# Optimization experiments

Hardware: AMD Instinct MI355X
Metric: run time of the kernel (lower is better)

## Reference

```python
import jax, jax.numpy as jnp
import numpy as np

N_NODES = 10000
N_EDGES = 160000
IN_FEATS = 512
H_FEATS = 512
NUM_CLASSES = 128


def setup_inputs() -> dict:
    key = jax.random.key(0)
    ks = jax.random.split(key, 7)
    h = jax.random.normal(ks[0], (N_NODES, IN_FEATS), dtype=jnp.float32)
    W1 = jax.random.normal(ks[1], (2 * IN_FEATS, H_FEATS), dtype=jnp.float32) * 0.02
    b1 = jax.random.normal(ks[2], (H_FEATS,), dtype=jnp.float32) * 0.02
    W2 = jax.random.normal(ks[3], (2 * H_FEATS, NUM_CLASSES), dtype=jnp.float32) * 0.02
    b2 = jax.random.normal(ks[4], (NUM_CLASSES,), dtype=jnp.float32) * 0.02
    src = jax.random.randint(ks[5], (N_EDGES,), 0, N_NODES, dtype=jnp.int32)
    dst = jax.random.randint(ks[6], (N_EDGES,), 0, N_NODES, dtype=jnp.int32)
    return {"h": h, "W1": W1, "b1": b1, "W2": W2, "b2": b2, "src": src, "dst": dst}


def _weighted_sage_conv(h, W, b, src, dst, n_nodes):
    # message = u_mul_e('h','w') with w == ones -> just gather source features
    msg = h[src]  # [E, d]
    # fn.mean reduce at destination: segment-sum / in-degree (0 if no in-edges)
    s = jax.ops.segment_sum(msg, dst, num_segments=n_nodes)  # [N, d]
    cnt = jax.ops.segment_sum(jnp.ones((src.shape[0],), h.dtype), dst, num_segments=n_nodes)
    h_N = s / jnp.maximum(cnt, 1.0)[:, None]
    h_total = jnp.concatenate([h, h_N], axis=1)  # [N, 2d]
    return h_total @ W + b


def reference(h, W1, b1, W2, b2, src, dst):
    n = h.shape[0]
    h1 = jax.nn.relu(_weighted_sage_conv(h, W1, b1, src, dst, n))
    return _weighted_sage_conv(h1, W2, b2, src, dst, n)
```

## Files before the change

### kernel.cpp

```cpp
#include <hip/hip_runtime.h>

typedef unsigned short u16;
typedef unsigned char u8;
typedef __attribute__((ext_vector_type(2))) float floatx2;
typedef __attribute__((ext_vector_type(4))) float floatx4;
typedef __attribute__((ext_vector_type(8))) __bf16 bf16x8;
typedef __attribute__((ext_vector_type(2))) unsigned short us2;
typedef __attribute__((ext_vector_type(4))) unsigned short us4;
typedef __attribute__((ext_vector_type(8))) unsigned short us8;
typedef __attribute__((ext_vector_type(2))) unsigned int u32x2;

static __device__ __forceinline__ float b2f(u16 v) {
    union { unsigned u; float f; } x; x.u = ((unsigned)v) << 16; return x.f;
}
static __device__ __forceinline__ u16 f2b(float f) {
    union { float f; unsigned u; } x; x.f = f;
    unsigned u = x.u;
    return (u16)((u + 0x7fffu + ((u >> 16) & 1u)) >> 16);
}

#define GLOAD_LDS16(g, l) __builtin_amdgcn_global_load_lds( \
    (const __attribute__((address_space(1))) void*)(g),     \
    (__attribute__((address_space(3))) void*)(l), 16, 0, 0)

#define CAP 64
#define SPILLMAX 4096

static __device__ __forceinline__ int detect_blk(const u16* __restrict__ p,
                                                 int nelem, int* sh) {
    if (threadIdx.x == 0) *sh = 0;
    __syncthreads();
    const int lim = nelem < 512 ? nelem : 512;
    int found = 0;
    for (int j = threadIdx.x; 2 * j < lim; j += 256) {
        unsigned v = p[2 * j] & 0x7fffu;
        if (v >= 0x4280u) found = 1;
    }
    if (found) atomicOr(sh, 1);
    __syncthreads();
    return *sh;
}

__global__ __launch_bounds__(256) void k_d1(
    const int* __restrict__ src, const int* __restrict__ dst, int E, int Nn,
    int* __restrict__ cnt, int* __restrict__ bucket,
    int* __restrict__ nspill, int* __restrict__ spill,
    const void* __restrict__ h, const void* __restrict__ W1,
    const void* __restrict__ b1, const void* __restrict__ W2,
    const void* __restrict__ b2,
    u16* __restrict__ Hb, u16* __restrict__ W1T, u16* __restrict__ W2T,
    u16* __restrict__ b1c, u16* __restrict__ b2c, int* __restrict__ flags,
    int nFill, int nHb) {
    __shared__ u16 tile[32][33];
    __shared__ int sh;
    const int b = blockIdx.x;
    const int t = threadIdx.x;

    if (b < nFill) {
        int e = b * 256 + t;
        if (e < E) {
            int d = dst[e], s = src[e];
            if ((unsigned)d < (unsigned)Nn && (unsigned)s < (unsigned)Nn) {
                int p = atomicAdd(&cnt[d], 1);
                if (p < CAP) bucket[d * CAP + p] = s;
                else {
                    int q = atomicAdd(nspill, 1);
                    if (q < SPILLMAX) { spill[2 * q] = d; spill[2 * q + 1] = s; }
                }
            }
        }
        return;
    }
    if (b < nFill + nHb) {
        const int f = detect_blk((const u16*)h, Nn * 512, &sh);
        int i = ((b - nFill) * 256 + t) * 8;
        if (i >= Nn * 512) return;
        if (f) {
            const float* s = (const float*)h;
            us8 o;
#pragma unroll
            for (int k = 0; k < 8; ++k) o[k] = f2b(s[i + k]);
            *(us8*)(Hb + i) = o;
        } else {
            *(us8*)(Hb + i) = *(const us8*)((const u16*)h + i);
        }
        return;
    }
    if (b < nFill + nHb + 512) {
        const int f = detect_blk((const u16*)W1, 1024 * 512, &sh);
        int sub = b - nFill - nHb;
        int half = sub >> 8, idx = sub & 255;
        const int bx = (idx & 15) * 32, by = (idx >> 4) * 32;
        const int koff = half * 512, noff = half * 512;
        const int tx = t & 31, ty = t >> 5;
        for (int i = ty; i < 32; i += 8) {
            long id = (long)(koff + by + i) * 512 + (bx + tx);
            tile[i][tx] = f ? f2b(((const float*)W1)[id]) : ((const u16*)W1)[id];
        }
        __syncthreads();
        for (int i = ty; i < 32; i += 8)
            W1T[(long)(noff + bx + i) * 512 + (by + tx)] = tile[tx][i];
        return;
    }
    if (b < nFill + nHb + 640) {
        const int f = detect_blk((const u16*)W2, 1024 * 128, &sh);
        int sub = b - nFill - nHb - 512;
        int half = sub >> 6, idx = sub & 63;
        const int bx = (idx & 3) * 32, by = (idx >> 2) * 32;
        const int koff = half * 512, noff = half * 128;
        const int tx = t & 31, ty = t >> 5;
        for (int i = ty; i < 32; i += 8) {
            long id = (long)(koff + by + i) * 128 + (bx + tx);
            tile[i][tx] = f ? f2b(((const float*)W2)[id]) : ((const u16*)W2)[id];
        }
        __syncthreads();
        for (int i = ty; i < 32; i += 8)
            W2T[(long)(noff + bx + i) * 512 + (by + tx)] = tile[tx][i];
        return;
    }
    {
        const int f1 = detect_blk((const u16*)b1, 512, &sh);
        for (int i = t; i < 512; i += 256)
            b1c[i] = f1 ? f2b(((const float*)b1)[i]) : ((const u16*)b1)[i];
        const int f2 = detect_blk((const u16*)b2, 128, &sh);
        if (t < 128)
            b2c[t] = f2 ? f2b(((const float*)b2)[t]) : ((const u16*)b2)[t];
        const int fh = detect_blk((const u16*)h, Nn * 512, &sh);
        if (t == 0) flags[0] = fh;
    }
}

__device__ __forceinline__ void gemm_acc256(const u16* __restrict__ A,
                                            const u16* __restrict__ Bt,
                                            long brow, int bobs,
                                            floatx4 acc[4][4], u16* lA, u16* lB) {
    const int tid = threadIdx.x;
    const int wv = tid >> 6;
    const int ln = tid & 63;
    const int lrow = ln >> 2;
    const int lk = (ln & 3) * 8;
    const int m0 = ln & 15;
    const int kq = (ln >> 4) * 8;
    const int wc = wv * 64;

#pragma unroll
    for (int i = 0; i < 4; ++i)
#pragma unroll
        for (int j = 0; j < 4; ++j) acc[i][j] = (floatx4){0.f, 0.f, 0.f, 0.f};

    for (int kt = 0; kt < 512; kt += 32) {
        GLOAD_LDS16(A + (brow + wv * 16 + lrow) * 512 + kt + lk, lA + wv * 512);
#pragma unroll
        for (int i = 0; i < 4; ++i) {
            const int c = i * 4 + wv;
            GLOAD_LDS16(Bt + (long)(bobs + c * 16 + lrow) * 512 + kt + lk, lB + c * 512);
        }
        __syncthreads();
        bf16x8 af[4], bf[4];
#pragma unroll
        for (int i = 0; i < 4; ++i)
            af[i] = *(const bf16x8*)(lA + (i * 16 + m0) * 32 + kq);
#pragma unroll
        for (int j = 0; j < 4; ++j)
            bf[j] = *(const bf16x8*)(lB + (wc + j * 16 + m0) * 32 + kq);
#pragma unroll
        for (int i = 0; i < 4; ++i)
#pragma unroll
            for (int j = 0; j < 4; ++j)
                acc[i][j] = __builtin_amdgcn_mfma_f32_16x16x32_bf16(af[i], bf[j],
                                                                    acc[i][j], 0, 0, 0);
        __syncthreads();
    }
}

__global__ __launch_bounds__(256) void k_gemm1_256(
    const u16* __restrict__ A, const u16* __restrict__ Bt,
    u16* __restrict__ C1s, u8* __restrict__ P1, int Mstore) {
    __shared__ __align__(16) u16 lA[64 * 32];
    __shared__ __align__(16) u16 lB[256 * 32];
    const int by = blockIdx.y;
    const int bcol = by * 256;
    const long brow = (long)blockIdx.x * 64;
    floatx4 acc[4][4];
    gemm_acc256(A, Bt, brow, bcol, acc, lA, lB);

    const int ln = threadIdx.x & 63;
    const int wv = threadIdx.x >> 6;
    const int wc = wv * 64;
    const int m0 = ln & 15;
    const int q4 = (ln >> 4) * 4;
    if (by < 2) {
#pragma unroll
        for (int i = 0; i < 4; ++i)
#pragma unroll
            for (int r = 0; r < 4; ++r) {
                long row = brow + i * 16 + q4 + r;
                if (row < Mstore) {
#pragma unroll
                    for (int j = 0; j < 4; ++j)
                        C1s[row * 512 + (bcol + wc + j * 16 + m0)] = f2b(acc[i][j][r]);
                }
            }
    } else {
        const int coff = bcol - 512;
#pragma unroll
        for (int i = 0; i < 4; ++i)
#pragma unroll
            for (int r = 0; r < 4; ++r) {
                long row = brow + i * 16 + q4 + r;
                if (row < Mstore) {
#pragma unroll
                    for (int j = 0; j < 4; ++j) {
                        float v = acc[i][j][r];
                        int pk = __builtin_amdgcn_cvt_pk_fp8_f32(v, v, 0, false);
                        P1[row * 512 + (coff + wc + j * 16 + m0)] = (u8)(pk & 0xff);
                    }
                }
            }
    }
}

__device__ __forceinline__ void gemm_acc64(const u16* __restrict__ A,
                                           const u16* __restrict__ Bt,
                                           long brow, int bobs,
                                           floatx4 acc[4][2], u16* lA, u16* lB) {
    const int tid = threadIdx.x;
    const int wv = tid >> 6;
    const int ln = tid & 63;
    const int lrow = ln >> 2;
    const int lk = (ln & 3) * 8;
    const int m0 = ln & 15;
    const int kq = (ln >> 4) * 8;
    const int wc = wv * 32;

#pragma unroll
    for (int i = 0; i < 4; ++i)
#pragma unroll
        for (int j = 0; j < 2; ++j) acc[i][j] = (floatx4){0.f, 0.f, 0.f, 0.f};

    for (int kt = 0; kt < 512; kt += 32) {
        GLOAD_LDS16(A + (brow + wv * 16 + lrow) * 512 + kt + lk, lA + wv * 512);
#pragma unroll
        for (int i = 0; i < 2; ++i) {
            const int c = i * 4 + wv;
            GLOAD_LDS16(Bt + (long)(bobs + c * 16 + lrow) * 512 + kt + lk, lB + c * 512);
        }
        __syncthreads();
        bf16x8 af[4], bf[2];
#pragma unroll
        for (int i = 0; i < 4; ++i)
            af[i] = *(const bf16x8*)(lA + (i * 16 + m0) * 32 + kq);
#pragma unroll
        for (int j = 0; j < 2; ++j)
            bf[j] = *(const bf16x8*)(lB + (wc + j * 16 + m0) * 32 + kq);
#pragma unroll
        for (int i = 0; i < 4; ++i)
#pragma unroll
            for (int j = 0; j < 2; ++j)
                acc[i][j] = __builtin_amdgcn_mfma_f32_16x16x32_bf16(af[i], bf[j],
                                                                    acc[i][j], 0, 0, 0);
        __syncthreads();
    }
}

__global__ __launch_bounds__(256) void k_gemm2_64(
    const u16* __restrict__ A, const u16* __restrict__ Bt,
    u16* __restrict__ C2s, u16* __restrict__ P2, int Mstore) {
    __shared__ __align__(16) u16 lA[64 * 32];
    __shared__ __align__(16) u16 lB[128 * 32];
    const long brow = (long)blockIdx.x * 64;
    floatx4 acc[4][2];
    gemm_acc64(A, Bt, brow, blockIdx.y * 128, acc, lA, lB);

    u16* C = blockIdx.y ? P2 : C2s;
    const int ln = threadIdx.x & 63;
    const int wv = threadIdx.x >> 6;
    const int wc = wv * 32;
    const int m0 = ln & 15;
    const int q4 = (ln >> 4) * 4;
#pragma unroll
    for (int i = 0; i < 4; ++i)
#pragma unroll
        for (int r = 0; r < 4; ++r) {
            long row = brow + i * 16 + q4 + r;
            if (row < Mstore) {
#pragma unroll
                for (int j = 0; j < 2; ++j)
                    C[row * 128 + (wc + j * 16 + m0)] = f2b(acc[i][j][r]);
            }
        }
}

__global__ __launch_bounds__(256) void agg_h1(const u8* __restrict__ P1,
                                              const u16* __restrict__ C1s,
                                              const u16* __restrict__ b1c,
                                              const int* __restrict__ cnt,
                                              const int* __restrict__ bucket,
                                              const int* __restrict__ nspill,
                                              const int* __restrict__ spill,
                                              u16* __restrict__ h1, int Nn) {
    const int n = blockIdx.x * 4 + (threadIdx.x >> 6);
    const int l = threadIdx.x & 63;
    if (n >= Nn) return;
    const int c = cnt[n];
    const int inb = c < CAP ? c : CAP;
    const int* bk = bucket + (long)n * CAP;
    float a0 = 0.f, a1 = 0.f, a2 = 0.f, a3 = 0.f;
    float a4 = 0.f, a5 = 0.f, a6 = 0.f, a7 = 0.f;
    int e = 0;
    for (; e + 7 < inb; e += 8) {
        u32x2 w[8];
#pragma unroll
        for (int q = 0; q < 8; ++q) {
            int s = bk[e + q];
            w[q] = *(const u32x2*)(P1 + (long)s * 512 + l * 8);
        }
#pragma unroll
        for (int q = 0; q < 8; ++q) {
            floatx2 f0 = __builtin_amdgcn_cvt_pk_f32_fp8(w[q][0], false);
            floatx2 f1 = __builtin_amdgcn_cvt_pk_f32_fp8(w[q][0], true);
            floatx2 f2 = __builtin_amdgcn_cvt_pk_f32_fp8(w[q][1], false);
            floatx2 f3 = __builtin_amdgcn_cvt_pk_f32_fp8(w[q][1], true);
            a0 += f0[0]; a1 += f0[1]; a2 += f1[0]; a3 += f1[1];
            a4 += f2[0]; a5 += f2[1]; a6 += f3[0]; a7 += f3[1];
        }
    }
    for (; e < inb; ++e) {
        int s = bk[e];
        u32x2 w = *(const u32x2*)(P1 + (long)s * 512 + l * 8);
        floatx2 f0 = __builtin_amdgcn_cvt_pk_f32_fp8(w[0], false);
        floatx2 f1 = __builtin_amdgcn_cvt_pk_f32_fp8(w[0], true);
        floatx2 f2 = __builtin_amdgcn_cvt_pk_f32_fp8(w[1], false);
        floatx2 f3 = __builtin_amdgcn_cvt_pk_f32_fp8(w[1], true);
        a0 += f0[0]; a1 += f0[1]; a2 += f1[0]; a3 += f1[1];
        a4 += f2[0]; a5 += f2[1]; a6 += f3[0]; a7 += f3[1];
    }
    const int ns = *nspill;
    if (ns > 0) {
        int lim = ns < SPILLMAX ? ns : SPILLMAX;
        for (int q = 0; q < lim; ++q) {
            if (spill[2 * q] == n) {
                int s = spill[2 * q + 1];
                u32x2 w = *(const u32x2*)(P1 + (long)s * 512 + l * 8);
                floatx2 f0 = __builtin_amdgcn_cvt_pk_f32_fp8(w[0], false);
                floatx2 f1 = __builtin_amdgcn_cvt_pk_f32_fp8(w[0], true);
                floatx2 f2 = __builtin_amdgcn_cvt_pk_f32_fp8(w[1], false);
                floatx2 f3 = __builtin_amdgcn_cvt_pk_f32_fp8(w[1], true);
                a0 += f0[0]; a1 += f0[1]; a2 += f1[0]; a3 += f1[1];
                a4 += f2[0]; a5 += f2[1]; a6 += f3[0]; a7 += f3[1];
            }
        }
    }
    float inv = 1.0f / (float)(c > 1 ? c : 1);
    us8 sf = *(const us8*)(C1s + (long)n * 512 + l * 8);
    us8 bv = *(const us8*)(b1c + l * 8);
    us8 o;
    o[0] = f2b(fmaxf(b2f(sf[0]) + a0 * inv + b2f(bv[0]), 0.f));
    o[1] = f2b(fmaxf(b2f(sf[1]) + a1 * inv + b2f(bv[1]), 0.f));
    o[2] = f2b(fmaxf(b2f(sf[2]) + a2 * inv + b2f(bv[2]), 0.f));
    o[3] = f2b(fmaxf(b2f(sf[3]) + a3 * inv + b2f(bv[3]), 0.f));
    o[4] = f2b(fmaxf(b2f(sf[4]) + a4 * inv + b2f(bv[4]), 0.f));
    o[5] = f2b(fmaxf(b2f(sf[5]) + a5 * inv + b2f(bv[5]), 0.f));
    o[6] = f2b(fmaxf(b2f(sf[6]) + a6 * inv + b2f(bv[6]), 0.f));
    o[7] = f2b(fmaxf(b2f(sf[7]) + a7 * inv + b2f(bv[7]), 0.f));
    *(us8*)(h1 + (long)n * 512 + l * 8) = o;
}

__global__ __launch_bounds__(256) void agg_out(const u16* __restrict__ P2,
                                               const u16* __restrict__ C2s,
                                               const u16* __restrict__ b2c,
                                               const int* __restrict__ cnt,
                                               const int* __restrict__ bucket,
                                               const int* __restrict__ nspill,
                                               const int* __restrict__ spill,
                                               void* __restrict__ outv, int Nn,
                                               const int* __restrict__ flags) {
    const int n = blockIdx.x * 4 + (threadIdx.x >> 6);
    const int l = threadIdx.x & 63;
    if (n >= Nn) return;
    const int c = cnt[n];
    const int inb = c < CAP ? c : CAP;
    const int* bk = bucket + (long)n * CAP;
    float a0 = 0.f, a1 = 0.f;
    int e = 0;
    for (; e + 3 < inb; e += 4) {
        int s0 = bk[e], s1 = bk[e + 1], s2 = bk[e + 2], s3 = bk[e + 3];
        us2 v0 = *(const us2*)(P2 + (long)s0 * 128 + l * 2);
        us2 v1 = *(const us2*)(P2 + (long)s1 * 128 + l * 2);
        us2 v2 = *(const us2*)(P2 + (long)s2 * 128 + l * 2);
        us2 v3 = *(const us2*)(P2 + (long)s3 * 128 + l * 2);
        a0 += (b2f(v0[0]) + b2f(v1[0])) + (b2f(v2[0]) + b2f(v3[0]));
        a1 += (b2f(v0[1]) + b2f(v1[1])) + (b2f(v2[1]) + b2f(v3[1]));
    }
    for (; e < inb; ++e) {
        int s0 = bk[e];
        us2 v0 = *(const us2*)(P2 + (long)s0 * 128 + l * 2);
        a0 += b2f(v0[0]); a1 += b2f(v0[1]);
    }
    const int ns = *nspill;
    if (ns > 0) {
        int lim = ns < SPILLMAX ? ns : SPILLMAX;
        for (int q = 0; q < lim; ++q) {
            if (spill[2 * q] == n) {
                int s0 = spill[2 * q + 1];
                us2 v0 = *(const us2*)(P2 + (long)s0 * 128 + l * 2);
                a0 += b2f(v0[0]); a1 += b2f(v0[1]);
            }
        }
    }
    float inv = 1.0f / (float)(c > 1 ? c : 1);
    us2 sf = *(const us2*)(C2s + (long)n * 128 + l * 2);
    us2 bv = *(const us2*)(b2c + l * 2);
    float o0 = b2f(sf[0]) + a0 * inv + b2f(bv[0]);
    float o1 = b2f(sf[1]) + a1 * inv + b2f(bv[1]);
    if (flags[0]) {
        float* o = (float*)outv + (long)n * 128 + l * 2;
        o[0] = o0; o[1] = o1;
    } else {
        us2 ob; ob[0] = f2b(o0); ob[1] = f2b(o1);
        *(us2*)((u16*)outv + (long)n * 128 + l * 2) = ob;
    }
}

extern "C" void kernel_launch(void* const* d_in, const int* in_sizes, int n_in,
                              void* d_out, int out_size, void* d_ws, size_t ws_size,
                              hipStream_t stream) {
    const int D = 512, NCLS = 128;
    const int Nn = in_sizes[0] / D;
    const int E  = in_sizes[5];
    const int mtiles = (Nn + 127) / 128;
    const int mt64 = (Nn + 63) / 64;
    const int Mpad = mtiles * 128;
    const int nFill = (E + 255) / 256;
    const int nHb = (Nn * D / 8 + 255) / 256;

    const int* src = (const int*)d_in[5];
    const int* dst = (const int*)d_in[6];

    char* p = (char*)d_ws;
    u16* Hb  = (u16*)p; p += (size_t)Mpad * D * 2;
    u16* h1  = (u16*)p; p += (size_t)Mpad * D * 2;
    u16* C1s = (u16*)p; p += (size_t)Mpad * D * 2;
    u8*  P1  = (u8*)p;  p += (size_t)Mpad * D;
    u16* C2s = (u16*)p; p += (size_t)Mpad * NCLS * 2;
    u16* P2  = (u16*)p; p += (size_t)Mpad * NCLS * 2;
    u16* W1T = (u16*)p; p += (size_t)1024 * D * 2;
    u16* W2T = (u16*)p; p += (size_t)256 * D * 2;
    u16* b1c = (u16*)p; p += 1024;
    u16* b2c = (u16*)p; p += 1024;
    int* flags  = (int*)p; p += 256;
    int* cnt    = (int*)p; p += (size_t)(Nn + 60) * 4;
    int* nspill = cnt + Nn;
    int* bucket = (int*)p; p += (size_t)Nn * CAP * 4;
    int* spill  = (int*)p; p += (size_t)SPILLMAX * 2 * 4;

    hipMemsetAsync(cnt, 0, (size_t)(Nn + 60) * 4, stream);

    k_d1<<<nFill + nHb + 641, 256, 0, stream>>>(
        src, dst, E, Nn, cnt, bucket, nspill, spill,
        d_in[0], d_in[1], d_in[2], d_in[3], d_in[4],
        Hb, W1T, W2T, b1c, b2c, flags, nFill, nHb);

    k_gemm1_256<<<dim3(mt64, 4), 256, 0, stream>>>(Hb, W1T, C1s, P1, Nn);

    agg_h1<<<(Nn + 3) / 4, 256, 0, stream>>>(P1, C1s, b1c, cnt, bucket,
                                             nspill, spill, h1, Nn);

    k_gemm2_64<<<dim3(mt64, 2), 256, 0, stream>>>(h1, W2T, C2s, P2, Nn);

    agg_out<<<(Nn + 3) / 4, 256, 0, stream>>>(P2, C2s, b2c, cnt, bucket,
                                              nspill, spill, d_out, Nn, flags);
}
```

Baseline: 158.7 us.

## Double-buffer GEMM LDS tiles, swizzle blocks across XCDs, add 4-edge gather tail

Both GEMM kernels now double-buffer their LDS tiles. The next k-slice is issued with global_load_lds while the current one is computed, synchronised by explicit vmcnt waits and barriers, so the two-barrier serial load-then-compute loop goes away. The block index is remapped so neighbouring tiles land on the same XCD, which should improve L2 reuse of A rows and B columns. The aggregation loop gains a 4-wide unrolled tail, cutting serial single-edge gathers. The cost is double the LDS per block, which may lower occupancy, and hand-tuned waitcnt values that must match the number of loads each wave issues.

Result: faster. 149.0 us (-6.1%).

```diff
diff --git a/kernel.cpp b/kernel.cpp
--- a/kernel.cpp
+++ b/kernel.cpp
@@ -39,6 +39,12 @@
     if (found) atomicOr(sh, 1);
     __syncthreads();
     return *sh;
+}
+
+static __device__ __forceinline__ int xcd_swz(int L, int nwg) {
+    const int q = nwg >> 3, r = nwg & 7;
+    const int x = L & 7, i = L >> 3;
+    return (x < r ? x * (q + 1) : r * (q + 1) + (x - r) * q) + i;
 }
 
 __global__ __launch_bounds__(256) void k_d1(
@@ -148,39 +154,62 @@
 #pragma unroll
         for (int j = 0; j < 4; ++j) acc[i][j] = (floatx4){0.f, 0.f, 0.f, 0.f};
 
-    for (int kt = 0; kt < 512; kt += 32) {
-        GLOAD_LDS16(A + (brow + wv * 16 + lrow) * 512 + kt + lk, lA + wv * 512);
-#pragma unroll
-        for (int i = 0; i < 4; ++i) {
-            const int c = i * 4 + wv;
-            GLOAD_LDS16(Bt + (long)(bobs + c * 16 + lrow) * 512 + kt + lk, lB + c * 512);
-        }
-        __syncthreads();
+    const u16* gA = A + (brow + wv * 16 + lrow) * 512 + lk;
+
+    auto STAGE = [&](int kt, int sel) {
+        u16* dA = lA + sel * 2048 + wv * 512;
+        u16* dB = lB + sel * 8192;
+        GLOAD_LDS16(gA + kt, dA);
+#pragma unroll
+        for (int ii = 0; ii < 4; ++ii) {
+            const int c = ii * 4 + wv;
+            GLOAD_LDS16(Bt + (long)(bobs + c * 16 + lrow) * 512 + kt + lk,
+                        dB + c * 512);
+        }
+    };
+    auto COMPUTE = [&](int sel) {
+        const u16* rA = lA + sel * 2048;
+        const u16* rB = lB + sel * 8192;
         bf16x8 af[4], bf[4];
 #pragma unroll
         for (int i = 0; i < 4; ++i)
-            af[i] = *(const bf16x8*)(lA + (i * 16 + m0) * 32 + kq);
+            af[i] = *(const bf16x8*)(rA + (i * 16 + m0) * 32 + kq);
 #pragma unroll
         for (int j = 0; j < 4; ++j)
-            bf[j] = *(const bf16x8*)(lB + (wc + j * 16 + m0) * 32 + kq);
+            bf[j] = *(const bf16x8*)(rB + (wc + j * 16 + m0) * 32 + kq);
 #pragma unroll
         for (int i = 0; i < 4; ++i)
 #pragma unroll
             for (int j = 0; j < 4; ++j)
                 acc[i][j] = __builtin_amdgcn_mfma_f32_16x16x32_bf16(af[i], bf[j],
                                                                     acc[i][j], 0, 0, 0);
-        __syncthreads();
-    }
+    };
+
+    STAGE(0, 0);
+    for (int t = 0; t < 15; ++t) {
+        const int sel = t & 1;
+        STAGE((t + 1) << 5, sel ^ 1);
+        asm volatile("s_waitcnt vmcnt(5)" ::: "memory");
+        __builtin_amdgcn_s_barrier();
+        COMPUTE(sel);
+        asm volatile("s_waitcnt lgkmcnt(0)" ::: "memory");
+        __builtin_amdgcn_s_barrier();
+    }
+    asm volatile("s_waitcnt vmcnt(0)" ::: "memory");
+    __builtin_amdgcn_s_barrier();
+    COMPUTE(1);
 }
 
 __global__ __launch_bounds__(256) void k_gemm1_256(
     const u16* __restrict__ A, const u16* __restrict__ Bt,
     u16* __restrict__ C1s, u8* __restrict__ P1, int Mstore) {
-    __shared__ __align__(16) u16 lA[64 * 32];
-    __shared__ __align__(16) u16 lB[256 * 32];
-    const int by = blockIdx.y;
+    __shared__ __align__(16) u16 lA[2 * 64 * 32];
+    __shared__ __align__(16) u16 lB[2 * 256 * 32];
+    const int L = blockIdx.y * gridDim.x + blockIdx.x;
+    const int T = xcd_swz(L, gridDim.x * gridDim.y);
+    const int by = T & 3;
     const int bcol = by * 256;
-    const long brow = (long)blockIdx.x * 64;
+    const long brow = (long)(T >> 2) * 64;
     floatx4 acc[4][4];
     gemm_acc256(A, Bt, brow, bcol, acc, lA, lB);
 
@@ -238,41 +267,65 @@
 #pragma unroll
         for (int j = 0; j < 2; ++j) acc[i][j] = (floatx4){0.f, 0.f, 0.f, 0.f};
 
-    for (int kt = 0; kt < 512; kt += 32) {
-        GLOAD_LDS16(A + (brow + wv * 16 + lrow) * 512 + kt + lk, lA + wv * 512);
-#pragma unroll
-        for (int i = 0; i < 2; ++i) {
-            const int c = i * 4 + wv;
-            GLOAD_LDS16(Bt + (long)(bobs + c * 16 + lrow) * 512 + kt + lk, lB + c * 512);
-        }
-        __syncthreads();
+    const u16* gA = A + (brow + wv * 16 + lrow) * 512 + lk;
+
+    auto STAGE = [&](int kt, int sel) {
+        u16* dA = lA + sel * 2048 + wv * 512;
+        u16* dB = lB + sel * 4096;
+        GLOAD_LDS16(gA + kt, dA);
+#pragma unroll
+        for (int ii = 0; ii < 2; ++ii) {
+            const int c = ii * 4 + wv;
+            GLOAD_LDS16(Bt + (long)(bobs + c * 16 + lrow) * 512 + kt + lk,
+                        dB + c * 512);
+        }
+    };
+    auto COMPUTE = [&](int sel) {
+        const u16* rA = lA + sel * 2048;
+        const u16* rB = lB + sel * 4096;
         bf16x8 af[4], bf[2];
 #pragma unroll
         for (int i = 0; i < 4; ++i)
-            af[i] = *(const bf16x8*)(lA + (i * 16 + m0) * 32 + kq);
+            af[i] = *(const bf16x8*)(rA + (i * 16 + m0) * 32 + kq);
 #pragma unroll
         for (int j = 0; j < 2; ++j)
-            bf[j] = *(const bf16x8*)(lB + (wc + j * 16 + m0) * 32 + kq);
+            bf[j] = *(const bf16x8*)(rB + (wc + j * 16 + m0) * 32 + kq);
 #pragma unroll
         for (int i = 0; i < 4; ++i)
 #pragma unroll
             for (int j = 0; j < 2; ++j)
                 acc[i][j] = __builtin_amdgcn_mfma_f32_16x16x32_bf16(af[i], bf[j],
                                                                     acc[i][j], 0, 0, 0);
-        __syncthreads();
-    }
+    };
+
+    STAGE(0, 0);
+    for (int t = 0; t < 15; ++t) {
+        const int sel = t & 1;
+        STAGE((t + 1) << 5, sel ^ 1);
+        asm volatile("s_waitcnt vmcnt(3)" ::: "memory");
+        __builtin_amdgcn_s_barrier();
+        COMPUTE(sel);
+        asm volatile("s_waitcnt lgkmcnt(0)" ::: "memory");
+        __builtin_amdgcn_s_barrier();
+    }
+    asm volatile("s_waitcnt vmcnt(0)" ::: "memory");
+    __builtin_amdgcn_s_barrier();
+    COMPUTE(1);
 }
 
 __global__ __launch_bounds__(256) void k_gemm2_64(
     const u16* __restrict__ A, const u16* __restrict__ Bt,
     u16* __restrict__ C2s, u16* __restrict__ P2, int Mstore) {
-    __shared__ __align__(16) u16 lA[64 * 32];
-    __shared__ __align__(16) u16 lB[128 * 32];
-    const long brow = (long)blockIdx.x * 64;
+    __shared__ __align__(16) u16 lA[2 * 64 * 32];
+    __shared__ __align__(16) u16 lB[2 * 128 * 32];
+    const int L = blockIdx.y * gridDim.x + blockIdx.x;
+    const int T = xcd_swz(L, gridDim.x * gridDim.y);
+    const int by = T & 1;
+    const long brow = (long)(T >> 1) * 64;
     floatx4 acc[4][2];
-    gemm_acc64(A, Bt, brow, blockIdx.y * 128, acc, lA, lB);
-
-    u16* C = blockIdx.y ? P2 : C2s;
+    gemm_acc64(A, Bt, brow, by * 128, acc, lA, lB);
+
+    u16* C = by ? P2 : C2s;
     const int ln = threadIdx.x & 63;
     const int wv = threadIdx.x >> 6;
     const int wc = wv * 32;
@@ -317,6 +370,23 @@
         }
 #pragma unroll
         for (int q = 0; q < 8; ++q) {
+            floatx2 f0 = __builtin_amdgcn_cvt_pk_f32_fp8(w[q][0], false);
+            floatx2 f1 = __builtin_amdgcn_cvt_pk_f32_fp8(w[q][0], true);
+            floatx2 f2 = __builtin_amdgcn_cvt_pk_f32_fp8(w[q][1], false);
+            floatx2 f3 = __builtin_amdgcn_cvt_pk_f32_fp8(w[q][1], true);
+            a0 += f0[0]; a1 += f0[1]; a2 += f1[0]; a3 += f1[1];
+            a4 += f2[0]; a5 += f2[1]; a6 += f3[0]; a7 += f3[1];
+        }
+    }
+    for (; e + 3 < inb; e += 4) {
+        u32x2 w[4];
+#pragma unroll
+        for (int q = 0; q < 4; ++q) {
+            int s = bk[e + q];
+            w[q] = *(const u32x2*)(P1 + (long)s * 512 + l * 8);
+        }
+#pragma unroll
+        for (int q = 0; q < 4; ++q) {
             floatx2 f0 = __builtin_amdgcn_cvt_pk_f32_fp8(w[q][0], false);
             floatx2 f1 = __builtin_amdgcn_cvt_pk_f32_fp8(w[q][0], true);
             floatx2 f2 = __builtin_amdgcn_cvt_pk_f32_fp8(w[q][1], false);
```
